# Optimization experiments

Measured on AMD Instinct MI355X. Metric: run time of the kernel, lower is better.

The kernel has to match this reference:

```python
import jax, jax.numpy as jnp
import numpy as np

HEADS = 8

def setup_inputs() -> dict:
    key = jax.random.key(0)
    ks = jax.random.split(key, 4)
    b, n, d = 4, 4097, 128  # n = 64*64 + 1 (CLS + spatial)
    x = jax.random.normal(ks[0], (b, n, d), dtype=jnp.float32)
    W_qkv = jax.random.normal(ks[1], (d, 3 * d), dtype=jnp.float32) * (d ** -0.5)
    b_qkv = jnp.zeros((3 * d,), dtype=jnp.float32)
    W_out = jax.random.normal(ks[2], (d, d), dtype=jnp.float32) * (d ** -0.5)
    b_out = jnp.zeros((d,), dtype=jnp.float32)
    return {"x": x, "W_qkv": W_qkv, "b_qkv": b_qkv, "W_out": W_out, "b_out": b_out}

def reference(x, W_qkv, b_qkv, W_out, b_out):
    b, n, d = x.shape
    h = HEADS
    dh = d // h
    scale = d ** -0.5  # note: module scales by dim**-0.5, not head_dim**-0.5
    qkv = x @ W_qkv + b_qkv                      # [b, n, 3d]
    q, k, v = jnp.split(qkv, 3, axis=-1)
    def to_heads(t):
        return t.reshape(b, n, h, dh).transpose(0, 2, 1, 3)  # [b, h, n, dh]
    q, k, v = to_heads(q), to_heads(k), to_heads(v)
    dots = jnp.einsum('bhid,bhjd->bhij', q, k) * scale       # [b, h, n, n]
    attn = jax.nn.softmax(dots, axis=-1)
    out = jnp.einsum('bhij,bhjd->bhid', attn, v)             # [b, h, n, dh]
    out = out.transpose(0, 2, 1, 3).reshape(b, n, d)
    return out @ W_out + b_out
```

## Files before the change

kernel.cpp:

```cpp
#include <hip/hip_runtime.h>
#include <hip/hip_bf16.h>
#include <stdint.h>


#define BB 4
#define NN 4097
#define NNP 4112
#define DD 128
#define HH 8
#define DH 16
#define BH (BB*HH)
#define ROWS (BB*NN)
#define MT  1025
#define NSP 4

typedef _Float16 h4 __attribute__((ext_vector_type(4)));
typedef _Float16 h8 __attribute__((ext_vector_type(8)));
typedef __fp16   fp16v2 __attribute__((ext_vector_type(2)));
typedef float    f4 __attribute__((ext_vector_type(4)));

#define QSCALE (0.08838834764831845f * 1.4426950408889634f)

#if __has_builtin(__builtin_amdgcn_exp2f)
#define EXP2F(x) __builtin_amdgcn_exp2f(x)
#else
#define EXP2F(x) exp2f(x)
#endif

union H4u { h4 v; fp16v2 p[2]; };
union H8u { h8 v; fp16v2 p[4]; };

static __device__ __forceinline__ H4u pack4u(float a, float b, float c, float d) {
    H4u u;
#if __has_builtin(__builtin_amdgcn_cvt_pkrtz)
    u.p[0] = __builtin_amdgcn_cvt_pkrtz(a, b);
    u.p[1] = __builtin_amdgcn_cvt_pkrtz(c, d);
#else
    u.v[0] = (_Float16)a; u.v[1] = (_Float16)b; u.v[2] = (_Float16)c; u.v[3] = (_Float16)d;
#endif
    return u;
}

static __device__ __forceinline__ h8 pack8u(const float4& t0, const float4& t1) {
    H8u u;
#if __has_builtin(__builtin_amdgcn_cvt_pkrtz)
    u.p[0] = __builtin_amdgcn_cvt_pkrtz(t0.x, t0.y);
    u.p[1] = __builtin_amdgcn_cvt_pkrtz(t0.z, t0.w);
    u.p[2] = __builtin_amdgcn_cvt_pkrtz(t1.x, t1.y);
    u.p[3] = __builtin_amdgcn_cvt_pkrtz(t1.z, t1.w);
#else
    u.v[0]=(_Float16)t0.x; u.v[1]=(_Float16)t0.y; u.v[2]=(_Float16)t0.z; u.v[3]=(_Float16)t0.w;
    u.v[4]=(_Float16)t1.x; u.v[5]=(_Float16)t1.y; u.v[6]=(_Float16)t1.z; u.v[7]=(_Float16)t1.w;
#endif
    return u.v;
}

__global__ __launch_bounds__(256) void prep(
    const float* __restrict__ Wqkv,
    const float* __restrict__ Wout,
    _Float16* __restrict__ WqkvT,
    _Float16* __restrict__ WoutT)
{
    const int id = blockIdx.x*256 + threadIdx.x;
    if (id < 384*128) {
        const int n = id >> 7, k = id & 127;
        const float s = (n < 128) ? QSCALE : 1.0f;
        WqkvT[id] = (_Float16)(Wqkv[k*384 + n] * s);
    } else if (id < 384*128 + 128*128) {
        const int e = id - 384*128;
        const int n = e >> 7, k = e & 127;
        WoutT[e] = (_Float16)(Wout[k*128 + n]);
    }
}

__global__ __launch_bounds__(256) void qkv_mfma(
    const float* __restrict__ x,
    const _Float16* __restrict__ WqkvT,
    const float* __restrict__ bqkv,
    _Float16* __restrict__ Qh,
    _Float16* __restrict__ Kh,
    _Float16* __restrict__ Vh)
{
    __shared__ _Float16 tile[16][392];
    const int wid  = blockIdx.x;
    const int wave = threadIdx.x >> 6;
    const int lane = threadIdx.x & 63;
    const int quad = lane >> 4, l16 = lane & 15;

    const int arow = wid*16 + l16;
    const int arc  = (arow < ROWS) ? arow : (ROWS - 1);
    const float* xr = x + (size_t)arc*DD;
    h8 af[4];
    #pragma unroll
    for (int kk = 0; kk < 4; ++kk) {
        const float4 t0 = *(const float4*)(xr + kk*32 + quad*8);
        const float4 t1 = *(const float4*)(xr + kk*32 + quad*8 + 4);
        af[kk] = pack8u(t0, t1);
    }

    const int nt0 = wave*6;

    for (int nt = nt0; nt < nt0 + 6; nt += 2) {
        const float b0 = bqkv[nt*16 + l16]      * ((nt   < 8) ? QSCALE : 1.0f);
        const float b1 = bqkv[nt*16 + 16 + l16] * ((nt+1 < 8) ? QSCALE : 1.0f);
        f4 a0 = {b0,b0,b0,b0}, a1 = {b1,b1,b1,b1};
        #pragma unroll
        for (int kk = 0; kk < 4; ++kk) {
            const h8 bf0 = *(const h8*)(WqkvT + (size_t)(nt*16      + l16)*DD + kk*32 + quad*8);
            const h8 bf1 = *(const h8*)(WqkvT + (size_t)(nt*16 + 16 + l16)*DD + kk*32 + quad*8);
            a0 = __builtin_amdgcn_mfma_f32_16x16x32_f16(af[kk], bf0, a0, 0, 0, 0);
            a1 = __builtin_amdgcn_mfma_f32_16x16x32_f16(af[kk], bf1, a1, 0, 0, 0);
        }
        #pragma unroll
        for (int u = 0; u < 2; ++u) {
            const int ntc = nt + u;
            const f4 av = u ? a1 : a0;
            #pragma unroll
            for (int r = 0; r < 4; ++r)
                tile[quad*4 + r][ntc*16 + l16] = (_Float16)av[r];
        }
    }
    __syncthreads();

    for (int u = threadIdx.x; u < 384; u += 256) {
        const int ntc = u >> 4, lt = u & 15;
        const int row = wid*16 + lt;
        if (row < ROWS) {
            const int which = ntc >> 3, head = ntc & 7;
            _Float16* base = (which == 0) ? Qh : ((which == 1) ? Kh : Vh);
            const int bidx = row / NN;
            const int nrow = row - bidx*NN;
            _Float16* dst = base + ((size_t)(bidx*HH + head)*NNP + nrow)*DH;
            *(h8*)dst       = *(const h8*)&tile[lt][ntc*16];
            *(h8*)(dst + 8) = *(const h8*)&tile[lt][ntc*16 + 8];
        }
    }
}

__global__ __launch_bounds__(256) void vt_transpose(
    const _Float16* __restrict__ Vh,
    _Float16* __restrict__ Vt)
{
    __shared__ _Float16 tile[128][DH + 2];
    const int tl  = blockIdx.x;
    const int bh  = blockIdx.y;
    const int tid = threadIdx.x;
    const int n0  = tl * 128;
    const int rem = (n0 + 128 <= NNP) ? 128 : (NNP - n0);

    {
        const int r  = tid >> 1;
        const int i8 = (tid & 1) * 8;
        const int rc = (r < rem) ? r : (rem - 1);
        const h8 v = *(const h8*)(Vh + ((size_t)bh*NNP + n0 + rc)*DH + i8);
        #pragma unroll
        for (int j = 0; j < 8; ++j) tile[r][i8 + j] = v[j];
    }
    __syncthreads();
    {
        const int i    = tid >> 4;
        const int nseg = tid & 15;
        if (nseg * 8 < rem) {
            h8 v;
            #pragma unroll
            for (int j = 0; j < 8; ++j) v[j] = tile[nseg*8 + j][i];
            *(h8*)(Vt + ((size_t)bh*DH + i)*NNP + n0 + nseg*8) = v;
        }
    }
}

__global__ __launch_bounds__(256, 8) void attn_mfma(
    const _Float16* __restrict__ Qh,
    const _Float16* __restrict__ Kh,
    const _Float16* __restrict__ Vt,
    _Float16* __restrict__ PACC,
    float* __restrict__ PL)
{
    const int qt   = blockIdx.x;
    const int bh   = blockIdx.y;
    const int sp   = blockIdx.z;
    const int tid  = threadIdx.x;
    const int wave = tid >> 6;
    const int lane = tid & 63;
    const int quad = lane >> 4;
    const int l16  = lane & 15;
    const int bidx = bh >> 3, head = bh & 7;

    const int qbase = qt*256 + wave*64;

    const _Float16* Qb = Qh + (size_t)bh*NNP*DH;
    h4 qf[4];
    #pragma unroll
    for (int g = 0; g < 4; ++g) {
        const int qr = qbase + g*16 + l16;
        const int qc = (qr < NN) ? qr : (NN-1);
        qf[g] = *(const h4*)(Qb + (size_t)qc*DH + quad*4);
    }

    f4 acc[4] = {{0,0,0,0},{0,0,0,0},{0,0,0,0},{0,0,0,0}};
    float ls[4] = {0.f,0.f,0.f,0.f};

    const int t0 = sp*64;
    const int t1 = t0 + 64;

    const _Float16* kp = Kh + ((size_t)bh*NNP + (size_t)t0*16 + l16)*DH + quad*4;
    const _Float16* vp = Vt + ((size_t)bh*DH + l16)*NNP + t0*16 + quad*4;

    h4 ak = *(const h4*)kp;
    h4 av = *(const h4*)vp;
    const f4 zero = {0.f,0.f,0.f,0.f};
#if __has_builtin(__builtin_amdgcn_fdot2)
    const fp16v2 one2 = {(__fp16)1.0f, (__fp16)1.0f};
#endif

    for (int tt = t0; tt < t1; ++tt) {
        kp += 16*DH; vp += 16;
        const h4 nak = *(const h4*)kp;
        const h4 nav = *(const h4*)vp;
        #pragma unroll
        for (int g = 0; g < 4; ++g) {
            f4 d = __builtin_amdgcn_mfma_f32_16x16x16f16(ak, qf[g], zero, 0, 0, 0);
            const float p0 = EXP2F(d[0]), p1 = EXP2F(d[1]), p2 = EXP2F(d[2]), p3 = EXP2F(d[3]);
            const H4u pb = pack4u(p0, p1, p2, p3);
#if __has_builtin(__builtin_amdgcn_fdot2)
            ls[g] = __builtin_amdgcn_fdot2(pb.p[0], one2,
                     __builtin_amdgcn_fdot2(pb.p[1], one2, ls[g], false), false);
#else
            ls[g] += (p0 + p1) + (p2 + p3);
#endif
            acc[g] = __builtin_amdgcn_mfma_f32_16x16x16f16(av, pb.v, acc[g], 0, 0, 0);
        }
        ak = nak; av = nav;
    }

    if (sp == 3) {
        #pragma unroll
        for (int g = 0; g < 4; ++g) {
            f4 d = __builtin_amdgcn_mfma_f32_16x16x16f16(ak, qf[g], zero, 0, 0, 0);
            const float p0 = (quad == 0) ? EXP2F(d[0]) : 0.f;
            ls[g] += p0;
            const H4u pb = pack4u(p0, 0.f, 0.f, 0.f);
            acc[g] = __builtin_amdgcn_mfma_f32_16x16x16f16(av, pb.v, acc[g], 0, 0, 0);
        }
    }

    const size_t rb = (size_t)sp*ROWS + (size_t)bidx*NN;
    #pragma unroll
    for (int g = 0; g < 4; ++g) {
        float l = ls[g];
        l += __shfl_xor(l, 16);
        l += __shfl_xor(l, 32);
        const int qr = qbase + g*16 + l16;
        if (qr < NN) {
            const float inv = 1.0f / l;
            const H4u st = pack4u(acc[g][0]*inv, acc[g][1]*inv, acc[g][2]*inv, acc[g][3]*inv);
            *(h4*)(PACC + (rb + qr)*DD + head*DH + quad*4) = st.v;
            if (quad == 0) PL[(rb + qr)*HH + head] = l;
        }
    }
}

__global__ __launch_bounds__(256, 1) void out_mfma(
    const _Float16* __restrict__ PACC,
    const float* __restrict__ PL,
    const _Float16* __restrict__ WoutT,
    const float* __restrict__ bout,
    float* __restrict__ out)
{
    const int wid  = blockIdx.x*4 + (threadIdx.x >> 6);
    if (wid >= MT) return;
    const int lane = threadIdx.x & 63;
    const int quad = lane >> 4, l16 = lane & 15;
    const int hq   = quad >> 1;

    const int arow = wid*16 + l16;
    const int arc  = (arow < ROWS) ? arow : (ROWS - 1);

    h8 pf[NSP][4]; float lv[NSP][4];
    #pragma unroll
    for (int sp = 0; sp < NSP; ++sp) {
        const _Float16* pb  = PACC + ((size_t)sp*ROWS + arc)*DD;
        const float*    plb = PL   + ((size_t)sp*ROWS + arc)*HH;
        #pragma unroll
        for (int kk = 0; kk < 4; ++kk) {
            pf[sp][kk] = *(const h8*)(pb + kk*32 + quad*8);
            lv[sp][kk] = plb[kk*2 + hq];
        }
    }
    h8 wf[4][2][4];
    #pragma unroll
    for (int p = 0; p < 4; ++p)
        #pragma unroll
        for (int u = 0; u < 2; ++u)
            #pragma unroll
            for (int kk = 0; kk < 4; ++kk)
                wf[p][u][kk] = *(const h8*)(WoutT + (size_t)((p*2+u)*16 + l16)*DD + kk*32 + quad*8);

    h8 af[4];
    #pragma unroll
    for (int kk = 0; kk < 4; ++kk) {
        float lsum = 0.f;
        #pragma unroll
        for (int sp = 0; sp < NSP; ++sp) lsum += lv[sp][kk];
        const float inv = 1.0f / lsum;
        H8u u;
        #pragma unroll
        for (int j = 0; j < 4; ++j) {
            float a = 0.f, b = 0.f;
            #pragma unroll
            for (int sp = 0; sp < NSP; ++sp) {
                const float s = lv[sp][kk]*inv;
                a += s*(float)pf[sp][kk][2*j];
                b += s*(float)pf[sp][kk][2*j+1];
            }
#if __has_builtin(__builtin_amdgcn_cvt_pkrtz)
            u.p[j] = __builtin_amdgcn_cvt_pkrtz(a, b);
#else
            u.v[2*j] = (_Float16)a; u.v[2*j+1] = (_Float16)b;
#endif
        }
        af[kk] = u.v;
    }

    const int r0 = wid*16 + quad*4;

    #pragma unroll
    for (int p = 0; p < 4; ++p) {
        const int nt = p*2;
        const float b0 = bout[nt*16 + l16];
        const float b1 = bout[nt*16 + 16 + l16];
        f4 a0 = {b0,b0,b0,b0}, a1 = {b1,b1,b1,b1};
        #pragma unroll
        for (int kk = 0; kk < 4; ++kk) {
            a0 = __builtin_amdgcn_mfma_f32_16x16x32_f16(af[kk], wf[p][0][kk], a0, 0, 0, 0);
            a1 = __builtin_amdgcn_mfma_f32_16x16x32_f16(af[kk], wf[p][1][kk], a1, 0, 0, 0);
        }
        #pragma unroll
        for (int r = 0; r < 4; ++r) {
            const int row = r0 + r;
            if (row < ROWS) {
                out[(size_t)row*DD + nt*16      + l16] = a0[r];
                out[(size_t)row*DD + nt*16 + 16 + l16] = a1[r];
            }
        }
    }
}

extern "C" void kernel_launch(void* const* d_in, const int* in_sizes, int n_in,
                              void* d_out, int out_size, void* d_ws, size_t ws_size,
                              hipStream_t stream) {
    const float* x    = (const float*)d_in[0];
    const float* Wqkv = (const float*)d_in[1];
    const float* bqkv = (const float*)d_in[2];
    const float* Wout = (const float*)d_in[3];
    const float* bout = (const float*)d_in[4];
    for (int i = 0; i < n_in; ++i) {
        switch (in_sizes[i]) {
            case 2097664: x    = (const float*)d_in[i]; break;
            case 49152:   Wqkv = (const float*)d_in[i]; break;
            case 384:     bqkv = (const float*)d_in[i]; break;
            case 16384:   Wout = (const float*)d_in[i]; break;
            case 128:     bout = (const float*)d_in[i]; break;
            default: break;
        }
    }
    float* out = (float*)d_out;

    const size_t perh = (size_t)BH * NNP * DH;
    _Float16* Qh   = (_Float16*)d_ws;
    _Float16* Kh   = Qh + perh;
    _Float16* Vt   = Kh + perh;
    _Float16* Vh   = Vt + perh;
    _Float16* PACC = Vh;
    float*    PL    = (float*)(PACC + (size_t)NSP*ROWS*DD);
    _Float16* WqkvT = (_Float16*)(PL + (size_t)NSP*ROWS*HH);
    _Float16* WoutT = WqkvT + 384*128;

    const int prep_total = 384*128 + 128*128;

    hipLaunchKernelGGL(prep, dim3((prep_total + 255)/256), dim3(256), 0, stream,
                       Wqkv, Wout, WqkvT, WoutT);
    hipLaunchKernelGGL(qkv_mfma, dim3(MT), dim3(256), 0, stream,
                       x, WqkvT, bqkv, Qh, Kh, Vh);
    hipLaunchKernelGGL(vt_transpose, dim3(33, BH), dim3(256), 0, stream,
                       Vh, Vt);
    hipLaunchKernelGGL(attn_mfma, dim3(17, BH, NSP), dim3(256), 0, stream,
                       Qh, Kh, Vt, PACC, PL);
    hipLaunchKernelGGL(out_mfma, dim3((MT + 3)/4), dim3(256), 0, stream,
                       PACC, PL, WoutT, bout, out);
}
```

Baseline: 179.4 us.

## Fuse V transpose into QKV kernel and restructure output projection per-wave

The QKV projection kernel now writes V directly in transposed layout to the Vt buffer, which removes the separate vt_transpose kernel launch and its extra global round trip. The output projection is also restructured: each block handles one 16-row tile, threads cooperatively merge the split-K partials into shared memory, and each wave computes two of the eight output column tiles. This raises the number of blocks and lowers per-thread register use. The cost is scattered 8-byte transposed stores for V, which may coalesce poorly, plus an extra LDS sync in the output kernel. The padded tail of Vt beyond row NN is no longer written by these kernels.

```diff
diff --git a/kernel.cpp b/kernel.cpp
--- a/kernel.cpp
+++ b/kernel.cpp
@@ -79,15 +79,20 @@
     const float* __restrict__ bqkv,
     _Float16* __restrict__ Qh,
     _Float16* __restrict__ Kh,
-    _Float16* __restrict__ Vh)
+    _Float16* __restrict__ Vt)
 {
-    __shared__ _Float16 tile[16][392];
+    __shared__ _Float16 tile[16][264];
     const int wid  = blockIdx.x;
     const int wave = threadIdx.x >> 6;
     const int lane = threadIdx.x & 63;
     const int quad = lane >> 4, l16 = lane & 15;
 
-    const int arow = wid*16 + l16;
+    const int rowlo = wid*16;
+    const int blo   = rowlo / NN;
+    const bool vfast = (rowlo + 15 < ROWS) && (rowlo + 15 - blo*NN < NN);
+    const int nrow0 = rowlo - blo*NN;
+
+    const int arow = rowlo + l16;
     const int arc  = (arow < ROWS) ? arow : (ROWS - 1);
     const float* xr = x + (size_t)arc*DD;
     h8 af[4];
@@ -115,56 +120,45 @@
         for (int u = 0; u < 2; ++u) {
             const int ntc = nt + u;
             const f4 av = u ? a1 : a0;
-            #pragma unroll
-            for (int r = 0; r < 4; ++r)
-                tile[quad*4 + r][ntc*16 + l16] = (_Float16)av[r];
+            if (ntc < 16) {
+                #pragma unroll
+                for (int r = 0; r < 4; ++r)
+                    tile[quad*4 + r][ntc*16 + l16] = (_Float16)av[r];
+            } else {
+                const int head = ntc & 7;
+                if (vfast) {
+                    h4 pk;
+                    pk[0] = (_Float16)av[0]; pk[1] = (_Float16)av[1];
+                    pk[2] = (_Float16)av[2]; pk[3] = (_Float16)av[3];
+                    *(h4*)(Vt + ((size_t)(blo*HH + head)*DH + l16)*NNP + nrow0 + quad*4) = pk;
+                } else {
+                    #pragma unroll
+                    for (int r = 0; r < 4; ++r) {
+                        const int row = rowlo + quad*4 + r;
+                        if (row < ROWS) {
+                            const int bidx = row / NN;
+                            const int nrow = row - bidx*NN;
+                            Vt[((size_t)(bidx*HH + head)*DH + l16)*NNP + nrow] = (_Float16)av[r];
+                        }
+                    }
+                }
+            }
         }
     }
     __syncthreads();
 
-    for (int u = threadIdx.x; u < 384; u += 256) {
+    {
+        const int u   = threadIdx.x;
         const int ntc = u >> 4, lt = u & 15;
-        const int row = wid*16 + lt;
+        const int row = rowlo + lt;
         if (row < ROWS) {
-            const int which = ntc >> 3, head = ntc & 7;
-            _Float16* base = (which == 0) ? Qh : ((which == 1) ? Kh : Vh);
+            _Float16* base = (ntc < 8) ? Qh : Kh;
+            const int head = ntc & 7;
             const int bidx = row / NN;
             const int nrow = row - bidx*NN;
             _Float16* dst = base + ((size_t)(bidx*HH + head)*NNP + nrow)*DH;
             *(h8*)dst       = *(const h8*)&tile[lt][ntc*16];
             *(h8*)(dst + 8) = *(const h8*)&tile[lt][ntc*16 + 8];
-        }
-    }
-}
-
-__global__ __launch_bounds__(256) void vt_transpose(
-    const _Float16* __restrict__ Vh,
-    _Float16* __restrict__ Vt)
-{
-    __shared__ _Float16 tile[128][DH + 2];
-    const int tl  = blockIdx.x;
-    const int bh  = blockIdx.y;
-    const int tid = threadIdx.x;
-    const int n0  = tl * 128;
-    const int rem = (n0 + 128 <= NNP) ? 128 : (NNP - n0);
-
-    {
-        const int r  = tid >> 1;
-        const int i8 = (tid & 1) * 8;
-        const int rc = (r < rem) ? r : (rem - 1);
-        const h8 v = *(const h8*)(Vh + ((size_t)bh*NNP + n0 + rc)*DH + i8);
-        #pragma unroll
-        for (int j = 0; j < 8; ++j) tile[r][i8 + j] = v[j];
-    }
-    __syncthreads();
-    {
-        const int i    = tid >> 4;
-        const int nseg = tid & 15;
-        if (nseg * 8 < rem) {
-            h8 v;
-            #pragma unroll
-            for (int j = 0; j < 8; ++j) v[j] = tile[nseg*8 + j][i];
-            *(h8*)(Vt + ((size_t)bh*DH + i)*NNP + n0 + nseg*8) = v;
         }
     }
 }
@@ -260,88 +254,83 @@
     }
 }
 
-__global__ __launch_bounds__(256, 1) void out_mfma(
+__global__ __launch_bounds__(256) void out_mfma(
     const _Float16* __restrict__ PACC,
     const float* __restrict__ PL,
     const _Float16* __restrict__ WoutT,
     const float* __restrict__ bout,
     float* __restrict__ out)
 {
-    const int wid  = blockIdx.x*4 + (threadIdx.x >> 6);
-    if (wid >= MT) return;
-    const int lane = threadIdx.x & 63;
+    __shared__ _Float16 afl[16][136];
+    const int wid  = blockIdx.x;
+    const int tid  = threadIdx.x;
+    const int wave = tid >> 6;
+    const int lane = tid & 63;
     const int quad = lane >> 4, l16 = lane & 15;
-    const int hq   = quad >> 1;
-
-    const int arow = wid*16 + l16;
-    const int arc  = (arow < ROWS) ? arow : (ROWS - 1);
-
-    h8 pf[NSP][4]; float lv[NSP][4];
-    #pragma unroll
-    for (int sp = 0; sp < NSP; ++sp) {
-        const _Float16* pb  = PACC + ((size_t)sp*ROWS + arc)*DD;
-        const float*    plb = PL   + ((size_t)sp*ROWS + arc)*HH;
-        #pragma unroll
-        for (int kk = 0; kk < 4; ++kk) {
-            pf[sp][kk] = *(const h8*)(pb + kk*32 + quad*8);
-            lv[sp][kk] = plb[kk*2 + hq];
-        }
-    }
-    h8 wf[4][2][4];
-    #pragma unroll
-    for (int p = 0; p < 4; ++p)
-        #pragma unroll
-        for (int u = 0; u < 2; ++u)
+    const int nt   = wave*2;
+
+    h8 wf[2][4];
+    #pragma unroll
+    for (int u = 0; u < 2; ++u)
+        #pragma unroll
+        for (int kk = 0; kk < 4; ++kk)
+            wf[u][kk] = *(const h8*)(WoutT + (size_t)((nt+u)*16 + l16)*DD + kk*32 + quad*8);
+    const float b0 = bout[nt*16 + l16];
+    const float b1 = bout[nt*16 + 16 + l16];
+
+    {
+        const int t   = tid >> 4;
+        const int seg = tid & 15;
+        const int head = seg >> 1;
+        const int arow = wid*16 + t;
+        const int arc  = (arow < ROWS) ? arow : (ROWS - 1);
+        float l[NSP], lsum = 0.f;
+        #pragma unroll
+        for (int sp = 0; sp < NSP; ++sp) {
+            l[sp] = PL[((size_t)sp*ROWS + arc)*HH + head];
+            lsum += l[sp];
+        }
+        const float inv = 1.0f / lsum;
+        float m[8] = {0,0,0,0,0,0,0,0};
+        #pragma unroll
+        for (int sp = 0; sp < NSP; ++sp) {
+            const float s = l[sp]*inv;
+            const h8 p = *(const h8*)(PACC + ((size_t)sp*ROWS + arc)*DD + seg*8);
             #pragma unroll
-            for (int kk = 0; kk < 4; ++kk)
-                wf[p][u][kk] = *(const h8*)(WoutT + (size_t)((p*2+u)*16 + l16)*DD + kk*32 + quad*8);
+            for (int j = 0; j < 8; ++j) m[j] += s*(float)p[j];
+        }
+        H8u u;
+#if __has_builtin(__builtin_amdgcn_cvt_pkrtz)
+        u.p[0] = __builtin_amdgcn_cvt_pkrtz(m[0], m[1]);
+        u.p[1] = __builtin_amdgcn_cvt_pkrtz(m[2], m[3]);
+        u.p[2] = __builtin_amdgcn_cvt_pkrtz(m[4], m[5]);
+        u.p[3] = __builtin_amdgcn_cvt_pkrtz(m[6], m[7]);
+#else
+        #pragma unroll
+        for (int j = 0; j < 8; ++j) u.v[j] = (_Float16)m[j];
+#endif
+        *(h8*)&afl[t][seg*8] = u.v;
+    }
+    __syncthreads();
 
     h8 af[4];
     #pragma unroll
+    for (int kk = 0; kk < 4; ++kk)
+        af[kk] = *(const h8*)&afl[l16][kk*32 + quad*8];
+
+    f4 a0 = {b0,b0,b0,b0}, a1 = {b1,b1,b1,b1};
+    #pragma unroll
     for (int kk = 0; kk < 4; ++kk) {
-        float lsum = 0.f;
-        #pragma unroll
-        for (int sp = 0; sp < NSP; ++sp) lsum += lv[sp][kk];
-        const float inv = 1.0f / lsum;
-        H8u u;
-        #pragma unroll
-        for (int j = 0; j < 4; ++j) {
-            float a = 0.f, b = 0.f;
-            #pragma unroll
-            for (int sp = 0; sp < NSP; ++sp) {
-                const float s = lv[sp][kk]*inv;
-                a += s*(float)pf[sp][kk][2*j];
-                b += s*(float)pf[sp][kk][2*j+1];
-            }
-#if __has_builtin(__builtin_amdgcn_cvt_pkrtz)
-            u.p[j] = __builtin_amdgcn_cvt_pkrtz(a, b);
-#else
-            u.v[2*j] = (_Float16)a; u.v[2*j+1] = (_Float16)b;
-#endif
-        }
-        af[kk] = u.v;
-    }
-
+        a0 = __builtin_amdgcn_mfma_f32_16x16x32_f16(af[kk], wf[0][kk], a0, 0, 0, 0);
+        a1 = __builtin_amdgcn_mfma_f32_16x16x32_f16(af[kk], wf[1][kk], a1, 0, 0, 0);
+    }
     const int r0 = wid*16 + quad*4;
-
-    #pragma unroll
-    for (int p = 0; p < 4; ++p) {
-        const int nt = p*2;
-        const float b0 = bout[nt*16 + l16];
-        const float b1 = bout[nt*16 + 16 + l16];
-        f4 a0 = {b0,b0,b0,b0}, a1 = {b1,b1,b1,b1};
-        #pragma unroll
-        for (int kk = 0; kk < 4; ++kk) {
-            a0 = __builtin_amdgcn_mfma_f32_16x16x32_f16(af[kk], wf[p][0][kk], a0, 0, 0, 0);
-            a1 = __builtin_amdgcn_mfma_f32_16x16x32_f16(af[kk], wf[p][1][kk], a1, 0, 0, 0);
-        }
-        #pragma unroll
-        for (int r = 0; r < 4; ++r) {
-            const int row = r0 + r;
-            if (row < ROWS) {
-                out[(size_t)row*DD + nt*16      + l16] = a0[r];
-                out[(size_t)row*DD + nt*16 + 16 + l16] = a1[r];
-            }
+    #pragma unroll
+    for (int r = 0; r < 4; ++r) {
+        const int row = r0 + r;
+        if (row < ROWS) {
+            out[(size_t)row*DD + nt*16      + l16] = a0[r];
+            out[(size_t)row*DD + nt*16 + 16 + l16] = a1[r];
         }
     }
 }
@@ -370,8 +359,7 @@
     _Float16* Qh   = (_Float16*)d_ws;
     _Float16* Kh   = Qh + perh;
     _Float16* Vt   = Kh + perh;
-    _Float16* Vh   = Vt + perh;
-    _Float16* PACC = Vh;
+    _Float16* PACC = Vt + perh;
     float*    PL    = (float*)(PACC + (size_t)NSP*ROWS*DD);
     _Float16* WqkvT = (_Float16*)(PL + (size_t)NSP*ROWS*HH);
     _Float16* WoutT = WqkvT + 384*128;
@@ -381,11 +369,9 @@
     hipLaunchKernelGGL(prep, dim3((prep_total + 255)/256), dim3(256), 0, stream,
                        Wqkv, Wout, WqkvT, WoutT);
     hipLaunchKernelGGL(qkv_mfma, dim3(MT), dim3(256), 0, stream,
-                       x, WqkvT, bqkv, Qh, Kh, Vh);
-    hipLaunchKernelGGL(vt_transpose, dim3(33, BH), dim3(256), 0, stream,
-                       Vh, Vt);
+                       x, WqkvT, bqkv, Qh, Kh, Vt);
     hipLaunchKernelGGL(attn_mfma, dim3(17, BH, NSP), dim3(256), 0, stream,
                        Qh, Kh, Vt, PACC, PL);
-    hipLaunchKernelGGL(out_mfma, dim3((MT + 3)/4), dim3(256), 0, stream,
+    hipLaunchKernelGGL(out_mfma, dim3(MT), dim3(256), 0, stream,
                        PACC, PL, WoutT, bout, out);
 }
```

New measurement: 176.2 us. About the same (-1.8%).
